# Optimization experiments

Measured on AMD Instinct MI355X. Metric: run time of the kernel, lower is better.

## Reference

```python
import jax, jax.numpy as jnp
import numpy as np
from functools import partial

B, T, D = 512, 128, 128
H = 256            # hidden_dim
K = 49             # output_dim (CRF label space)
L = 7              # output_seq_length
LSTM_OUT = 2 * H   # bidirectional


def setup_inputs() -> dict:
    key = jax.random.key(0)
    ks = jax.random.split(key, 16)
    s = 0.1
    inp = {
        'x': jax.random.normal(ks[0], (B, T, D), jnp.float32),
        'labels': jax.random.randint(ks[1], (B, L), 0, K, jnp.int64),
        # LSTM forward direction (gate order i,f,g,o as in PyTorch); biases combined (b_ih+b_hh)
        'w_ih_f': jax.random.normal(ks[2], (4 * H, D), jnp.float32) * s,
        'w_hh_f': jax.random.normal(ks[3], (4 * H, H), jnp.float32) * s,
        'b_f': jax.random.normal(ks[4], (4 * H,), jnp.float32) * s,
        # LSTM backward direction
        'w_ih_b': jax.random.normal(ks[5], (4 * H, D), jnp.float32) * s,
        'w_hh_b': jax.random.normal(ks[6], (4 * H, H), jnp.float32) * s,
        'b_b': jax.random.normal(ks[7], (4 * H,), jnp.float32) * s,
        # attention MLP: Linear(2H -> H) -> tanh -> Linear(H -> 1)
        'aw1': jax.random.normal(ks[8], (H, LSTM_OUT), jnp.float32) * s,
        'ab1': jnp.zeros((H,), jnp.float32),
        'aw2': jax.random.normal(ks[9], (1, H), jnp.float32) * s,
        'ab2': jnp.zeros((1,), jnp.float32),
        # fc: Linear(2H -> K*L)
        'fc_w': jax.random.normal(ks[10], (K * L, LSTM_OUT), jnp.float32) * s,
        'fc_b': jnp.zeros((K * L,), jnp.float32),
        # CRF params
        'start_t': jax.random.normal(ks[11], (K,), jnp.float32) * s,
        'trans': jax.random.normal(ks[12], (K, K), jnp.float32) * s,
        'end_t': jax.random.normal(ks[13], (K,), jnp.float32) * s,
    }
    return inp


def _lstm_dir(x_tbd, w_ih, w_hh, b):
    # x_tbd: [T, B, D] -> hidden states [T, B, H]
    xw = jnp.einsum('tbd,gd->tbg', x_tbd, w_ih) + b  # precompute input projections
    h0 = jnp.zeros((x_tbd.shape[1], w_hh.shape[1]), x_tbd.dtype)
    c0 = jnp.zeros_like(h0)

    def step(carry, xw_t):
        h, c = carry
        gates = xw_t + h @ w_hh.T
        i, f, g, o = jnp.split(gates, 4, axis=-1)
        c = jax.nn.sigmoid(f) * c + jax.nn.sigmoid(i) * jnp.tanh(g)
        h = jax.nn.sigmoid(o) * jnp.tanh(c)
        return (h, c), h

    _, hs = jax.lax.scan(step, (h0, c0), xw)
    return hs


def _crf_loss(em, labels, start_t, trans, end_t):
    # em: [B, L, K]; full mask (all timesteps valid)
    # --- log partition via forward algorithm ---
    alpha0 = start_t + em[:, 0]  # [B, K]

    def step(alpha, em_t):
        alpha = jax.nn.logsumexp(alpha[:, :, None] + trans[None], axis=1) + em_t
        return alpha, None

    alpha, _ = jax.lax.scan(step, alpha0, jnp.swapaxes(em[:, 1:], 0, 1))
    logZ = jax.nn.logsumexp(alpha + end_t, axis=1)  # [B]
    # --- gold path score ---
    em_score = jnp.take_along_axis(em, labels[:, :, None], axis=2).squeeze(-1).sum(axis=1)
    trans_score = trans[labels[:, :-1], labels[:, 1:]].sum(axis=1)
    score = start_t[labels[:, 0]] + em_score + trans_score + end_t[labels[:, -1]]
    return -(score - logZ).mean()


def reference(x, labels, w_ih_f, w_hh_f, b_f, w_ih_b, w_hh_b, b_b,
              aw1, ab1, aw2, ab2, fc_w, fc_b, start_t, trans, end_t):
    labels = labels.astype(jnp.int32)
    x_t = jnp.swapaxes(x, 0, 1)  # [T, B, D]
    h_fwd = _lstm_dir(x_t, w_ih_f, w_hh_f, b_f)                    # [T, B, H]
    h_bwd = _lstm_dir(x_t[::-1], w_ih_b, w_hh_b, b_b)[::-1]        # [T, B, H]
    lstm_out = jnp.swapaxes(jnp.concatenate([h_fwd, h_bwd], axis=-1), 0, 1)  # [B, T, 2H]
    # dropout is identity at inference (eval mode)
    # attention pooling over time
    a = jnp.tanh(jnp.einsum('bte,he->bth', lstm_out, aw1) + ab1)
    scores = jnp.einsum('bth,oh->bto', a, aw2) + ab2               # [B, T, 1]
    attn = jax.nn.softmax(scores, axis=1)
    features = jnp.einsum('bto,bte->be', attn, lstm_out)           # [B, 2H]
    logits = (features @ fc_w.T + fc_b).reshape(-1, L, K)          # emissions [B, L, K]
    return _crf_loss(logits, labels, start_t, trans, end_t)
```

## Files before the change

### kernel.cpp

```cpp
#include <hip/hip_runtime.h>
#include <math.h>

#define B_SZ 512
#define T_SZ 128
#define D_SZ 128
#define H_SZ 256
#define K_SZ 49
#define L_SZ 7
#define E_SZ 512

typedef float f32x4 __attribute__((ext_vector_type(4)));
typedef short bf16x8 __attribute__((ext_vector_type(8)));

__device__ __forceinline__ unsigned short f2bf(float f) {
    union { float f; unsigned u; } v; v.f = f;
    unsigned r = v.u + 0x7FFFu + ((v.u >> 16) & 1u);
    return (unsigned short)(r >> 16);
}
__device__ __forceinline__ float bf2f(unsigned short h) {
    union { unsigned u; float f; } v; v.u = ((unsigned)h) << 16;
    return v.f;
}
__device__ __forceinline__ float fsigm(float x) {
    return __fdividef(1.0f, 1.0f + __expf(-x));
}
__device__ __forceinline__ float ftanh(float x) {
    x = fminf(fmaxf(x, -20.0f), 20.0f);
    float e = __expf(2.0f * x);
    return __fdividef(e - 1.0f, e + 1.0f);
}
__device__ __forceinline__ unsigned char f2fp8(float v) {
    int p = __builtin_amdgcn_cvt_pk_fp8_f32(v, 0.f, 0, false);
    return (unsigned char)(p & 0xff);
}

__global__ __launch_bounds__(256) void prep_w(
    const float* __restrict__ w_ih_f, const float* __restrict__ w_hh_f,
    const float* __restrict__ b_f, const float* __restrict__ w_ih_b,
    const float* __restrict__ w_hh_b, const float* __restrict__ b_b,
    unsigned char* __restrict__ Wt, float* __restrict__ bp)
{
    int idx = blockIdx.x * 256 + threadIdx.x;
    int e  = idx & 7;
    int cu = (idx >> 3) & 127;
    int hi = (idx >> 10) & 3;
    int rest = idx >> 12;
    int kk = rest % 12;
    int dw = rest / 12;
    int wv = dw & 7, dir = dw >> 3;
    int f = cu >> 4, u = cu & 15;
    int q = f >> 2, g = f & 3;
    int j = wv * 32 + q * 16 + u;
    int row = g * H_SZ + j;
    int k = kk * 32 + hi * 8 + e;
    const float* w_ih = dir ? w_ih_b : w_ih_f;
    const float* w_hh = dir ? w_hh_b : w_hh_f;
    float v = (k < H_SZ) ? w_hh[row * H_SZ + k] : w_ih[row * D_SZ + (k - H_SZ)];
    Wt[idx] = f2fp8(v);
    if (kk == 0 && hi == 0 && e == 0)
        bp[dw * 128 + cu] = (dir ? b_b : b_f)[row];
}

__global__ __launch_bounds__(256) void prep_aw(
    const float* __restrict__ aw1, short* __restrict__ aw1b)
{
    int idx = blockIdx.x * 256 + threadIdx.x;
    if (idx < H_SZ * E_SZ) aw1b[idx] = (short)f2bf(aw1[idx]);
}

__global__ __launch_bounds__(256) void xprep(
    const float* __restrict__ x, unsigned char* __restrict__ xb)
{
    size_t i = ((size_t)blockIdx.x * 256 + threadIdx.x) * 4;
    float4 v = *reinterpret_cast<const float4*>(x + i);
    int p0 = __builtin_amdgcn_cvt_pk_fp8_f32(v.x, v.y, 0, false);
    int p1 = __builtin_amdgcn_cvt_pk_fp8_f32(v.z, v.w, 0, false);
    unsigned w = (unsigned)(p0 & 0xffff) | ((unsigned)p1 << 16);
    *reinterpret_cast<unsigned*>(xb + i) = w;
}

__global__ __launch_bounds__(512, 2) void recur_kernel(
    const unsigned char* __restrict__ xb, const unsigned char* __restrict__ Wt,
    const float* __restrict__ bp, unsigned short* __restrict__ hb)
{
    const int dir = blockIdx.x & 1;
    const int b0 = (blockIdx.x >> 1) * 16;
    const int wv = threadIdx.x >> 6;
    const int l  = threadIdx.x & 63;
    const int u = l & 15, hi = l >> 4;

    __shared__ unsigned char hs[2][16][264];
    __shared__ unsigned char xs[16][136];

    for (int i = threadIdx.x; i < 16 * 264 * 1 / 4; i += 512)
        reinterpret_cast<unsigned*>(&hs[0][0][0])[i] = 0u;

    const unsigned char* wb = Wt + (size_t)(dir * 8 + wv) * 49152 + hi * 1024 + u * 8;
    long wreg[12][8];
    #pragma unroll
    for (int kk = 0; kk < 12; ++kk)
        #pragma unroll
        for (int f = 0; f < 8; ++f)
            wreg[kk][f] = *reinterpret_cast<const long*>(wb + kk * 4096 + f * 128);

    float bias[8];
    #pragma unroll
    for (int f = 0; f < 8; ++f)
        bias[f] = bp[(dir * 8 + wv) * 128 + f * 16 + u];

    const int xrow = threadIdx.x >> 5;
    const int xc = (threadIdx.x & 31) * 4;
    const unsigned char* xp = xb + ((size_t)(b0 + xrow) * T_SZ + (dir ? T_SZ - 1 : 0)) * D_SZ + xc;
    const int xstep = dir ? -D_SZ : D_SZ;
    unsigned xreg = *reinterpret_cast<const unsigned*>(xp);

    float c[2][4] = {};
    int cur = 0;

    for (int s = 0; s < T_SZ; ++s) {
        const int t = dir ? (T_SZ - 1 - s) : s;

        __syncthreads();
        *reinterpret_cast<unsigned*>(&xs[xrow][xc]) = xreg;
        if (s + 1 < T_SZ) { xp += xstep; xreg = *reinterpret_cast<const unsigned*>(xp); }
        __syncthreads();

        f32x4 acc[8];
        #pragma unroll
        for (int f = 0; f < 8; ++f)
            acc[f] = (f32x4){bias[f], bias[f], bias[f], bias[f]};

        #pragma unroll
        for (int kk = 0; kk < 12; ++kk) {
            long a = (kk < 8)
                ? *reinterpret_cast<const long*>(&hs[cur][u][kk * 32 + hi * 8])
                : *reinterpret_cast<const long*>(&xs[u][(kk - 8) * 32 + hi * 8]);
            #pragma unroll
            for (int f = 0; f < 8; ++f)
                acc[f] = __builtin_amdgcn_mfma_f32_16x16x32_fp8_fp8(a, wreg[kk][f], acc[f], 0, 0, 0);
        }

        #pragma unroll
        for (int q = 0; q < 2; ++q) {
            const int j = wv * 32 + q * 16 + u;
            #pragma unroll
            for (int r = 0; r < 4; ++r) {
                float iv = fsigm(acc[q * 4 + 0][r]);
                float fv = fsigm(acc[q * 4 + 1][r]);
                float gv = ftanh(acc[q * 4 + 2][r]);
                float ov = fsigm(acc[q * 4 + 3][r]);
                float cn = fv * c[q][r] + iv * gv;
                c[q][r] = cn;
                float h = ov * ftanh(cn);
                int row = hi * 4 + r;
                hs[cur ^ 1][row][j] = f2fp8(h);
                hb[((size_t)t * B_SZ + b0 + row) * E_SZ + dir * H_SZ + j] = f2bf(h);
            }
        }
        cur ^= 1;
    }
}

__global__ __launch_bounds__(256) void attn_mfma(
    const unsigned short* __restrict__ hb, const short* __restrict__ aw1b,
    const float* __restrict__ ab1, const float* __restrict__ aw2,
    float* __restrict__ scores)
{
    const int mt = blockIdx.x >> 1, nt = blockIdx.x & 1;
    const int r0 = mt * 128, n0 = nt * 128;
    const int tid = threadIdx.x;
    const int wv = tid >> 6, l = tid & 63, u = l & 15, hi = l >> 4;
    const int mw = wv >> 1, nw = wv & 1;

    __shared__ unsigned short As[128][40];
    __shared__ unsigned short Bs[128][40];

    f32x4 acc[4][4];
    #pragma unroll
    for (int m = 0; m < 4; ++m)
        #pragma unroll
        for (int n = 0; n < 4; ++n)
            acc[m][n] = (f32x4){0.f, 0.f, 0.f, 0.f};

    const int srow = tid >> 1;
    const int sc0 = (tid & 1) * 16;

    for (int k0 = 0; k0 < E_SZ; k0 += 32) {
        bf16x8 va0 = *reinterpret_cast<const bf16x8*>(hb + (size_t)(r0 + srow) * E_SZ + k0 + sc0);
        bf16x8 va1 = *reinterpret_cast<const bf16x8*>(hb + (size_t)(r0 + srow) * E_SZ + k0 + sc0 + 8);
        bf16x8 vb0 = *reinterpret_cast<const bf16x8*>(aw1b + (size_t)(n0 + srow) * E_SZ + k0 + sc0);
        bf16x8 vb1 = *reinterpret_cast<const bf16x8*>(aw1b + (size_t)(n0 + srow) * E_SZ + k0 + sc0 + 8);
        __syncthreads();
        *reinterpret_cast<bf16x8*>(&As[srow][sc0])     = va0;
        *reinterpret_cast<bf16x8*>(&As[srow][sc0 + 8]) = va1;
        *reinterpret_cast<bf16x8*>(&Bs[srow][sc0])     = vb0;
        *reinterpret_cast<bf16x8*>(&Bs[srow][sc0 + 8]) = vb1;
        __syncthreads();

        bf16x8 af[4], bf[4];
        #pragma unroll
        for (int m = 0; m < 4; ++m)
            af[m] = *reinterpret_cast<const bf16x8*>(&As[mw * 64 + m * 16 + u][hi * 8]);
        #pragma unroll
        for (int n = 0; n < 4; ++n)
            bf[n] = *reinterpret_cast<const bf16x8*>(&Bs[nw * 64 + n * 16 + u][hi * 8]);
        #pragma unroll
        for (int m = 0; m < 4; ++m)
            #pragma unroll
            for (int n = 0; n < 4; ++n)
                acc[m][n] = __builtin_amdgcn_mfma_f32_16x16x32_bf16(af[m], bf[n], acc[m][n], 0, 0, 0);
    }

    float t1[4], t2[4];
    #pragma unroll
    for (int n = 0; n < 4; ++n) {
        int h = n0 + nw * 64 + n * 16 + u;
        t1[n] = ab1[h]; t2[n] = aw2[h];
    }
    #pragma unroll
    for (int m = 0; m < 4; ++m) {
        #pragma unroll
        for (int r = 0; r < 4; ++r) {
            float s = 0.f;
            #pragma unroll
            for (int n = 0; n < 4; ++n)
                s += tanhf(acc[m][n][r] + t1[n]) * t2[n];
            #pragma unroll
            for (int o = 1; o < 16; o <<= 1) s += __shfl_xor(s, o);
            if (u == 0)
                atomicAdd(&scores[r0 + mw * 64 + m * 16 + hi * 4 + r], s);
        }
    }
}

__global__ __launch_bounds__(256) void attn_pool(
    const float* __restrict__ scores, const unsigned short* __restrict__ hb,
    float* __restrict__ features)
{
    int b = blockIdx.x;
    int tid = threadIdx.x;
    __shared__ float w[T_SZ];
    __shared__ float smax[4], ssum[4];

    float sc = (tid < T_SZ) ? scores[(size_t)tid * B_SZ + b] : -INFINITY;
    float m = sc;
    for (int o = 32; o; o >>= 1) m = fmaxf(m, __shfl_xor(m, o));
    if ((tid & 63) == 0) smax[tid >> 6] = m;
    __syncthreads();
    float M = fmaxf(fmaxf(smax[0], smax[1]), fmaxf(smax[2], smax[3]));
    float e = (tid < T_SZ) ? expf(sc - M) : 0.f;
    float se = e;
    for (int o = 32; o; o >>= 1) se += __shfl_xor(se, o);
    if ((tid & 63) == 0) ssum[tid >> 6] = se;
    __syncthreads();
    float S = ssum[0] + ssum[1] + ssum[2] + ssum[3];
    if (tid < T_SZ) w[tid] = e / S;
    __syncthreads();

    for (int e0 = tid; e0 < E_SZ; e0 += 256) {
        float acc = 0.f;
        for (int t = 0; t < T_SZ; ++t)
            acc += w[t] * bf2f(hb[((size_t)t * B_SZ + b) * E_SZ + e0]);
        features[(size_t)b * E_SZ + e0] = acc;
    }
}

__global__ __launch_bounds__(256) void fc_kernel(
    const float* __restrict__ features, const float* __restrict__ fc_w,
    const float* __restrict__ fc_b, float* __restrict__ logits)
{
    int bb = blockIdx.x * 8;
    int tid = threadIdx.x;
    __shared__ float f[8][E_SZ];
    for (int i = tid; i < 8 * E_SZ; i += 256)
        f[i >> 9][i & 511] = features[(size_t)(bb + (i >> 9)) * E_SZ + (i & 511)];
    __syncthreads();
    for (int o = tid; o < K_SZ * L_SZ; o += 256) {
        const float* wr = fc_w + (size_t)o * E_SZ;
        float acc[8];
        float bv = fc_b[o];
        #pragma unroll
        for (int b = 0; b < 8; ++b) acc[b] = bv;
        for (int e0 = 0; e0 < E_SZ; ++e0) {
            float wv = wr[e0];
            #pragma unroll
            for (int b = 0; b < 8; ++b) acc[b] += f[b][e0] * wv;
        }
        #pragma unroll
        for (int b = 0; b < 8; ++b)
            logits[(size_t)(bb + b) * (K_SZ * L_SZ) + o] = acc[b];
    }
}

__global__ __launch_bounds__(64) void crf_kernel(
    const float* __restrict__ logits, const int* __restrict__ labels,
    const float* __restrict__ start_t, const float* __restrict__ trans,
    const float* __restrict__ end_t, float* __restrict__ per_loss)
{
    int b = blockIdx.x;
    int tid = threadIdx.x;
    __shared__ float tr[K_SZ * K_SZ];
    __shared__ float em[K_SZ * L_SZ];
    __shared__ float alpha[K_SZ];

    for (int i = tid; i < K_SZ * K_SZ; i += 64) tr[i] = trans[i];
    for (int i = tid; i < K_SZ * L_SZ; i += 64)
        em[i] = logits[(size_t)b * (K_SZ * L_SZ) + i];
    __syncthreads();
    if (tid < K_SZ) alpha[tid] = start_t[tid] + em[tid];
    __syncthreads();

    for (int t = 1; t < L_SZ; ++t) {
        float na = 0.f;
        if (tid < K_SZ) {
            float m = -INFINITY;
            for (int k = 0; k < K_SZ; ++k)
                m = fmaxf(m, alpha[k] + tr[k * K_SZ + tid]);
            float s = 0.f;
            for (int k = 0; k < K_SZ; ++k)
                s += expf(alpha[k] + tr[k * K_SZ + tid] - m);
            na = m + logf(s) + em[t * K_SZ + tid];
        }
        __syncthreads();
        if (tid < K_SZ) alpha[tid] = na;
        __syncthreads();
    }

    float v = (tid < K_SZ) ? alpha[tid] + end_t[tid] : -INFINITY;
    float m = v;
    for (int o = 32; o; o >>= 1) m = fmaxf(m, __shfl_xor(m, o));
    float e = (tid < K_SZ) ? expf(v - m) : 0.f;
    for (int o = 32; o; o >>= 1) e += __shfl_xor(e, o);
    float logZ = m + logf(e);

    if (tid == 0) {
        const int* lab = labels + (size_t)b * L_SZ;
        float score = start_t[lab[0]] + end_t[lab[L_SZ - 1]];
        for (int t = 0; t < L_SZ; ++t) score += em[t * K_SZ + lab[t]];
        for (int t = 0; t < L_SZ - 1; ++t) score += tr[lab[t] * K_SZ + lab[t + 1]];
        per_loss[b] = logZ - score;
    }
}

__global__ __launch_bounds__(256) void reduce_kernel(
    const float* __restrict__ per_loss, float* __restrict__ out)
{
    int tid = threadIdx.x;
    float s = per_loss[tid] + per_loss[tid + 256];
    for (int o = 32; o; o >>= 1) s += __shfl_xor(s, o);
    __shared__ float part[4];
    if ((tid & 63) == 0) part[tid >> 6] = s;
    __syncthreads();
    if (tid == 0) out[0] = (part[0] + part[1] + part[2] + part[3]) / (float)B_SZ;
}

extern "C" void kernel_launch(void* const* d_in, const int* in_sizes, int n_in,
                              void* d_out, int out_size, void* d_ws, size_t ws_size,
                              hipStream_t stream)
{
    const float* x      = (const float*)d_in[0];
    const int*   labels = (const int*)d_in[1];
    const float* w_ih_f = (const float*)d_in[2];
    const float* w_hh_f = (const float*)d_in[3];
    const float* b_f    = (const float*)d_in[4];
    const float* w_ih_b = (const float*)d_in[5];
    const float* w_hh_b = (const float*)d_in[6];
    const float* b_b    = (const float*)d_in[7];
    const float* aw1    = (const float*)d_in[8];
    const float* ab1    = (const float*)d_in[9];
    const float* aw2    = (const float*)d_in[10];
    const float* fc_w   = (const float*)d_in[12];
    const float* fc_b   = (const float*)d_in[13];
    const float* start_t = (const float*)d_in[14];
    const float* trans   = (const float*)d_in[15];
    const float* end_t   = (const float*)d_in[16];
    float* out = (float*)d_out;

    char* ws = (char*)d_ws;
    size_t off = 0;
    unsigned char* Wt = (unsigned char*)(ws + off); off += (size_t)786432;
    float* bp        = (float*)(ws + off); off += (size_t)16 * 128 * 4;
    short* aw1b      = (short*)(ws + off); off += (size_t)H_SZ * E_SZ * 2;
    unsigned char* xb = (unsigned char*)(ws + off); off += (size_t)B_SZ * T_SZ * D_SZ;
    unsigned short* hb = (unsigned short*)(ws + off); off += (size_t)T_SZ * B_SZ * E_SZ * 2;
    float* scores    = (float*)(ws + off); off += (size_t)T_SZ * B_SZ * 4;
    float* features  = (float*)(ws + off); off += (size_t)B_SZ * E_SZ * 4;
    float* logits    = (float*)(ws + off); off += (size_t)B_SZ * K_SZ * L_SZ * 4;
    float* per_loss  = (float*)(ws + off); off += (size_t)B_SZ * 4;

    prep_w<<<3072, 256, 0, stream>>>(
        w_ih_f, w_hh_f, b_f, w_ih_b, w_hh_b, b_b, Wt, bp);
    prep_aw<<<(H_SZ * E_SZ + 255) / 256, 256, 0, stream>>>(aw1, aw1b);
    xprep<<<(B_SZ * T_SZ * D_SZ / 4 + 255) / 256, 256, 0, stream>>>(x, xb);

    hipMemsetAsync(scores, 0, (size_t)T_SZ * B_SZ * 4, stream);

    recur_kernel<<<64, 512, 0, stream>>>(xb, Wt, bp, hb);

    attn_mfma<<<1024, 256, 0, stream>>>(hb, aw1b, ab1, aw2, scores);

    attn_pool<<<B_SZ, 256, 0, stream>>>(scores, hb, features);

    fc_kernel<<<64, 256, 0, stream>>>(features, fc_w, fc_b, logits);

    crf_kernel<<<B_SZ, 64, 0, stream>>>(logits, labels, start_t, trans, end_t, per_loss);

    reduce_kernel<<<1, 256, 0, stream>>>(per_loss, out);
}
```

Before: 969.9 us.

## Split recurrent LSTM work across 16 waves per block and double-buffer x

The recurrent kernel now uses 1024 threads (16 waves) per block, each wave owning 16 hidden units instead of 32, so each wave holds half as many weight registers and issues half the MFMAs per step. The x-slice staging in shared memory is double-buffered, which removes one of the two barriers per timestep. Weight prep and bias layout are reordered to match the new per-wave mapping. The gain comes from more waves sharing the serial per-step latency, at the cost of more lanes contending at the block barrier and higher register pressure per SIMD.

```diff
diff --git a/kernel.cpp b/kernel.cpp
--- a/kernel.cpp
+++ b/kernel.cpp
@@ -42,15 +42,14 @@
 {
     int idx = blockIdx.x * 256 + threadIdx.x;
     int e  = idx & 7;
-    int cu = (idx >> 3) & 127;
-    int hi = (idx >> 10) & 3;
-    int rest = idx >> 12;
+    int u  = (idx >> 3) & 15;
+    int g  = (idx >> 7) & 3;
+    int hi = (idx >> 9) & 3;
+    int rest = idx >> 11;
     int kk = rest % 12;
     int dw = rest / 12;
-    int wv = dw & 7, dir = dw >> 3;
-    int f = cu >> 4, u = cu & 15;
-    int q = f >> 2, g = f & 3;
-    int j = wv * 32 + q * 16 + u;
+    int wv = dw & 15, dir = dw >> 4;
+    int j = wv * 16 + u;
     int row = g * H_SZ + j;
     int k = kk * 32 + hi * 8 + e;
     const float* w_ih = dir ? w_ih_b : w_ih_f;
@@ -58,7 +57,7 @@
     float v = (k < H_SZ) ? w_hh[row * H_SZ + k] : w_ih[row * D_SZ + (k - H_SZ)];
     Wt[idx] = f2fp8(v);
     if (kk == 0 && hi == 0 && e == 0)
-        bp[dw * 128 + cu] = (dir ? b_b : b_f)[row];
+        bp[(dw * 4 + g) * 16 + u] = (dir ? b_b : b_f)[row];
 }
 
 __global__ __launch_bounds__(256) void prep_aw(
@@ -79,7 +78,7 @@
     *reinterpret_cast<unsigned*>(xb + i) = w;
 }
 
-__global__ __launch_bounds__(512, 2) void recur_kernel(
+__global__ __launch_bounds__(1024) void recur_kernel(
     const unsigned char* __restrict__ xb, const unsigned char* __restrict__ Wt,
     const float* __restrict__ bp, unsigned short* __restrict__ hb)
 {
@@ -90,73 +89,79 @@
     const int u = l & 15, hi = l >> 4;
 
     __shared__ unsigned char hs[2][16][264];
-    __shared__ unsigned char xs[16][136];
-
-    for (int i = threadIdx.x; i < 16 * 264 * 1 / 4; i += 512)
+    __shared__ unsigned char xs[2][16][136];
+
+    for (int i = threadIdx.x; i < 1056; i += 1024)
         reinterpret_cast<unsigned*>(&hs[0][0][0])[i] = 0u;
 
-    const unsigned char* wb = Wt + (size_t)(dir * 8 + wv) * 49152 + hi * 1024 + u * 8;
-    long wreg[12][8];
+    const int dw = dir * 16 + wv;
+    const unsigned char* wb = Wt + (size_t)dw * 24576 + hi * 512 + u * 8;
+    long wreg[12][4];
     #pragma unroll
     for (int kk = 0; kk < 12; ++kk)
         #pragma unroll
-        for (int f = 0; f < 8; ++f)
-            wreg[kk][f] = *reinterpret_cast<const long*>(wb + kk * 4096 + f * 128);
-
-    float bias[8];
+        for (int g = 0; g < 4; ++g)
+            wreg[kk][g] = *reinterpret_cast<const volatile long*>(wb + kk * 2048 + g * 128);
+
+    float bias[4];
     #pragma unroll
-    for (int f = 0; f < 8; ++f)
-        bias[f] = bp[(dir * 8 + wv) * 128 + f * 16 + u];
-
-    const int xrow = threadIdx.x >> 5;
-    const int xc = (threadIdx.x & 31) * 4;
-    const unsigned char* xp = xb + ((size_t)(b0 + xrow) * T_SZ + (dir ? T_SZ - 1 : 0)) * D_SZ + xc;
-    const int xstep = dir ? -D_SZ : D_SZ;
-    unsigned xreg = *reinterpret_cast<const unsigned*>(xp);
-
-    float c[2][4] = {};
+    for (int g = 0; g < 4; ++g)
+        bias[g] = bp[(dw * 4 + g) * 16 + u];
+
+    const int xrow = threadIdx.x >> 6;
+    const int xoff = (threadIdx.x & 63) * 2;
+    const unsigned char* xbase = xb + (size_t)(b0 + xrow) * T_SZ * D_SZ + xoff;
+    const int tstep = dir ? -1 : 1;
+    const int t0 = dir ? (T_SZ - 1) : 0;
+    *reinterpret_cast<unsigned short*>(&xs[0][xrow][xoff]) =
+        *reinterpret_cast<const unsigned short*>(xbase + (size_t)t0 * D_SZ);
+    unsigned short xreg = *reinterpret_cast<const unsigned short*>(
+        xbase + (size_t)(t0 + tstep) * D_SZ);
+
+    const int j = wv * 16 + u;
+    float c[4] = {0.f, 0.f, 0.f, 0.f};
     int cur = 0;
+    __syncthreads();
 
     for (int s = 0; s < T_SZ; ++s) {
         const int t = dir ? (T_SZ - 1 - s) : s;
 
-        __syncthreads();
-        *reinterpret_cast<unsigned*>(&xs[xrow][xc]) = xreg;
-        if (s + 1 < T_SZ) { xp += xstep; xreg = *reinterpret_cast<const unsigned*>(xp); }
-        __syncthreads();
-
-        f32x4 acc[8];
-        #pragma unroll
-        for (int f = 0; f < 8; ++f)
-            acc[f] = (f32x4){bias[f], bias[f], bias[f], bias[f]};
+        if (s + 1 < T_SZ) {
+            *reinterpret_cast<unsigned short*>(&xs[(s + 1) & 1][xrow][xoff]) = xreg;
+            if (s + 2 < T_SZ)
+                xreg = *reinterpret_cast<const unsigned short*>(
+                    xbase + (size_t)(t + 2 * tstep) * D_SZ);
+        }
+
+        f32x4 acc[4];
+        #pragma unroll
+        for (int g = 0; g < 4; ++g)
+            acc[g] = (f32x4){bias[g], bias[g], bias[g], bias[g]};
 
         #pragma unroll
         for (int kk = 0; kk < 12; ++kk) {
             long a = (kk < 8)
                 ? *reinterpret_cast<const long*>(&hs[cur][u][kk * 32 + hi * 8])
-                : *reinterpret_cast<const long*>(&xs[u][(kk - 8) * 32 + hi * 8]);
+                : *reinterpret_cast<const long*>(&xs[s & 1][u][(kk - 8) * 32 + hi * 8]);
             #pragma unroll
-            for (int f = 0; f < 8; ++f)
-                acc[f] = __builtin_amdgcn_mfma_f32_16x16x32_fp8_fp8(a, wreg[kk][f], acc[f], 0, 0, 0);
-        }
-
-        #pragma unroll
-        for (int q = 0; q < 2; ++q) {
-            const int j = wv * 32 + q * 16 + u;
-            #pragma unroll
-            for (int r = 0; r < 4; ++r) {
-                float iv = fsigm(acc[q * 4 + 0][r]);
-                float fv = fsigm(acc[q * 4 + 1][r]);
-                float gv = ftanh(acc[q * 4 + 2][r]);
-                float ov = fsigm(acc[q * 4 + 3][r]);
-                float cn = fv * c[q][r] + iv * gv;
-                c[q][r] = cn;
-                float h = ov * ftanh(cn);
-                int row = hi * 4 + r;
-                hs[cur ^ 1][row][j] = f2fp8(h);
-                hb[((size_t)t * B_SZ + b0 + row) * E_SZ + dir * H_SZ + j] = f2bf(h);
-            }
-        }
+            for (int g = 0; g < 4; ++g)
+                acc[g] = __builtin_amdgcn_mfma_f32_16x16x32_fp8_fp8(a, wreg[kk][g], acc[g], 0, 0, 0);
+        }
+
+        #pragma unroll
+        for (int r = 0; r < 4; ++r) {
+            float iv = fsigm(acc[0][r]);
+            float fv = fsigm(acc[1][r]);
+            float gv = ftanh(acc[2][r]);
+            float ov = fsigm(acc[3][r]);
+            float cn = fv * c[r] + iv * gv;
+            c[r] = cn;
+            float h = ov * ftanh(cn);
+            int row = hi * 4 + r;
+            hs[cur ^ 1][row][j] = f2fp8(h);
+            hb[((size_t)t * B_SZ + b0 + row) * E_SZ + dir * H_SZ + j] = f2bf(h);
+        }
+        __syncthreads();
         cur ^= 1;
     }
 }
@@ -379,7 +384,7 @@
     char* ws = (char*)d_ws;
     size_t off = 0;
     unsigned char* Wt = (unsigned char*)(ws + off); off += (size_t)786432;
-    float* bp        = (float*)(ws + off); off += (size_t)16 * 128 * 4;
+    float* bp        = (float*)(ws + off); off += (size_t)2048 * 4;
     short* aw1b      = (short*)(ws + off); off += (size_t)H_SZ * E_SZ * 2;
     unsigned char* xb = (unsigned char*)(ws + off); off += (size_t)B_SZ * T_SZ * D_SZ;
     unsigned short* hb = (unsigned short*)(ws + off); off += (size_t)T_SZ * B_SZ * E_SZ * 2;
@@ -395,7 +400,7 @@
 
     hipMemsetAsync(scores, 0, (size_t)T_SZ * B_SZ * 4, stream);
 
-    recur_kernel<<<64, 512, 0, stream>>>(xb, Wt, bp, hb);
+    recur_kernel<<<64, 1024, 0, stream>>>(xb, Wt, bp, hb);
 
     attn_mfma<<<1024, 256, 0, stream>>>(hb, aw1b, ab1, aw2, scores);
 
```

Result: slower. 1.079 ms (+11.3%).
